# Kernel tuning notes

Measured on AMD Instinct MI355X. Metric: run time of the kernel, lower is better.

Reference implementation:

```python
import jax, jax.numpy as jnp
import numpy as np

# static config (matches init_kwargs / input_specs)
B, S, D, H, DH = 4, 2048, 2048, 16, 128
MAX_LEN = 1024  # round_up_to_multiple_of_256(max ragged length); lengths below max at 1024
ROPE_BASE = 10000.0


def setup_inputs() -> dict:
    key = jax.random.key(0)
    ks = jax.random.split(key, 8)
    q_src = jax.random.normal(ks[0], (B, MAX_LEN, D), jnp.float32)
    k_src = jax.random.normal(ks[1], (B, S, D), jnp.float32)
    v_src = jax.random.normal(ks[2], (B, S, D), jnp.float32)
    std = 1.0 / np.sqrt(D)
    Wq = jax.random.normal(ks[3], (D, H * DH), jnp.float32) * std
    Wk = jax.random.normal(ks[4], (D, H * DH), jnp.float32) * std
    Wv = jax.random.normal(ks[5], (D, H * DH), jnp.float32) * std
    Wo = jax.random.normal(ks[6], (H * DH, D), jnp.float32) * (1.0 / np.sqrt(H * DH))
    # mask[0]: causal bool [B,S,S]; mask[1]: full position ids [B,S]
    mask0 = jnp.broadcast_to(jnp.tril(jnp.ones((S, S), bool)), (B, S, S))
    pos_full = jnp.broadcast_to(jnp.arange(S, dtype=jnp.int32), (B, S))
    # ragged skip_mask: row i keeps lengths[i] random positions (max 1024 -> MAX_LEN)
    lengths = jnp.array([1024, 896, 768, 640], jnp.int32)
    scores = jax.random.uniform(ks[7], (B, S))
    ranks = jnp.argsort(jnp.argsort(scores, axis=1), axis=1)
    skip_mask = ranks < lengths[:, None]
    return {"q_src": q_src, "k_src": k_src, "v_src": v_src,
            "Wq": Wq, "Wk": Wk, "Wv": Wv, "Wo": Wo,
            "mask0": mask0, "pos_full": pos_full, "skip_mask": skip_mask}


def _rope(x, positions):
    # x: [B,H,L,DH], positions: [B,L] int -> rotary embedding on full head dim
    dh = x.shape[-1]
    inv_freq = 1.0 / (ROPE_BASE ** (jnp.arange(0, dh, 2, dtype=jnp.float32) / dh))
    freqs = positions.astype(jnp.float32)[:, :, None] * inv_freq      # [B,L,dh/2]
    emb = jnp.concatenate([freqs, freqs], axis=-1)[:, None]           # [B,1,L,dh]
    x1, x2 = jnp.split(x, 2, axis=-1)
    rot = jnp.concatenate([-x2, x1], axis=-1)                         # rotate_half
    return x * jnp.cos(emb) + rot * jnp.sin(emb)


def reference(q_src, k_src, v_src, Wq, Wk, Wv, Wo, mask0, pos_full, skip_mask):
    def heads(x, W):
        y = x @ W
        return y.reshape(x.shape[0], x.shape[1], H, DH).transpose(0, 2, 1, 3)

    q = heads(q_src, Wq)   # [B,H,MAX_LEN,DH]
    k = heads(k_src, Wk)   # [B,H,S,DH]
    v = heads(v_src, Wv)   # [B,H,S,DH]

    # _trim_attention_mask: gather kept rows (True-first, stable order), pad to MAX_LEN
    order = jnp.argsort(jnp.where(skip_mask, 0, 1), axis=1)[:, :MAX_LEN]  # [B,MAX_LEN]
    n = skip_mask.sum(axis=1)                                             # ragged lengths
    valid = jnp.arange(MAX_LEN)[None, :] < n[:, None]                     # [B,MAX_LEN]
    amask = jnp.take_along_axis(mask0, order[:, :, None], axis=1) & valid[:, :, None]
    pos_trim = jnp.where(valid, jnp.take_along_axis(pos_full, order, axis=1), 0)

    # RoPE: trimmed positions for q, full positions for k
    q = _rope(q, pos_trim)
    k = _rope(k, pos_full)

    # masked SDPA; fully-masked (padded) query rows -> zero output
    logits = jnp.einsum('bhld,bhsd->bhls', q, k) / np.sqrt(DH).astype(np.float32)
    logits = jnp.where(amask[:, None], logits, jnp.finfo(logits.dtype).min)
    probs = jax.nn.softmax(logits, axis=-1) * valid[:, None, :, None]
    ctx = jnp.einsum('bhls,bhsd->bhld', probs, v)                         # [B,H,MAX_LEN,DH]

    out = ctx.transpose(0, 2, 1, 3).reshape(B, MAX_LEN, H * DH) @ Wo     # [B,MAX_LEN,D]
    return out
```

## Files before the change

### kernel.cpp

```cpp
#include <hip/hip_runtime.h>

#define BB 4
#define SS 2048
#define DD 2048
#define HH 16
#define DHD 128
#define MAXL 1024

typedef __bf16 bf16x8 __attribute__((ext_vector_type(8)));
typedef float f32x4 __attribute__((ext_vector_type(4)));
typedef unsigned int u32_as1 __attribute__((address_space(1)));
typedef unsigned int u32_as3 __attribute__((address_space(3)));

__device__ __forceinline__ unsigned short f2bf(float f) {
  unsigned int u = __builtin_bit_cast(unsigned int, f);
  u += 0x7fffu + ((u >> 16) & 1u);
  return (unsigned short)(u >> 16);
}
__device__ __forceinline__ float bf2f(unsigned short h) {
  unsigned int u = ((unsigned int)h) << 16;
  return __builtin_bit_cast(float, u);
}
union U4 { uint4 u; bf16x8 b; };
__device__ __forceinline__ bf16x8 ldfrag(const unsigned short* p) {
  U4 x; x.u = *(const uint4*)p; return x.b;
}
__device__ __forceinline__ void gl_lds16(const void* g, void* l) {
  __builtin_amdgcn_global_load_lds((const u32_as1*)g, (u32_as3*)l, 16, 0, 0);
}

template <int C>
__device__ __forceinline__ float dppf(float x) {
  return __builtin_bit_cast(float,
      __builtin_amdgcn_mov_dpp(__builtin_bit_cast(int, x), C, 0xF, 0xF, true));
}
__device__ __forceinline__ float rmax16(float x) {
  x = fmaxf(x, dppf<0xB1>(x));
  x = fmaxf(x, dppf<0x4E>(x));
  x = fmaxf(x, dppf<0x141>(x));
  x = fmaxf(x, dppf<0x140>(x));
  return x;
}
__device__ __forceinline__ float radd16(float x) {
  x += dppf<0xB1>(x);
  x += dppf<0x4E>(x);
  x += dppf<0x141>(x);
  x += dppf<0x140>(x);
  return x;
}

#define NCVT 40960
#define NTW  4096
__global__ __launch_bounds__(256) void prep(
    const float* __restrict__ q, const float* __restrict__ k, const float* __restrict__ v,
    unsigned short* __restrict__ oq, unsigned short* __restrict__ ok,
    unsigned short* __restrict__ ov,
    const float* __restrict__ w0, const float* __restrict__ w1,
    const float* __restrict__ w2, const float* __restrict__ w3,
    unsigned short* __restrict__ t0, unsigned short* __restrict__ t1,
    unsigned short* __restrict__ t2, unsigned short* __restrict__ t3,
    const int* __restrict__ skip, int* __restrict__ posk, int* __restrict__ nval) {
  __shared__ __align__(16) unsigned short tile[64 * 76];
  __shared__ int cnts[64], offs[64];
  const int bid = blockIdx.x;
  const int tx = threadIdx.x;

  if (bid < NCVT) {
    const int nq = BB * MAXL * DD / 4, nk = BB * SS * DD / 4;
    int idx = bid * 256 + tx;
    const float* src; unsigned short* dst; int off;
    if (idx < nq) { src = q; dst = oq; off = idx; }
    else if (idx < nq + nk) { src = k; dst = ok; off = idx - nq; }
    else { src = v; dst = ov; off = idx - nq - nk; }
    float4 vv = ((const float4*)src)[off];
    ushort4 hh;
    hh.x = f2bf(vv.x); hh.y = f2bf(vv.y); hh.z = f2bf(vv.z); hh.w = f2bf(vv.w);
    ((ushort4*)dst)[off] = hh;
  } else if (bid < NCVT + NTW) {
    int rem = bid - NCVT;
    int z = rem >> 10, r2 = rem & 1023;
    int bx = r2 & 31, by = r2 >> 5;
    const float* W; unsigned short* Wt;
    switch (z) {
      case 0: W = w0; Wt = t0; break;
      case 1: W = w1; Wt = t1; break;
      case 2: W = w2; Wt = t2; break;
      default: W = w3; Wt = t3; break;
    }
    int K0 = by * 64, N0 = bx * 64;
    #pragma unroll
    for (int i = 0; i < 4; i++) {
      int r = (tx >> 4) + i * 16, c4 = (tx & 15) * 4;
      float4 vv = *(const float4*)&W[(size_t)(K0 + r) * DD + N0 + c4];
      ushort4 hh;
      hh.x = f2bf(vv.x); hh.y = f2bf(vv.y); hh.z = f2bf(vv.z); hh.w = f2bf(vv.w);
      *(ushort4*)&tile[r * 76 + c4] = hh;
    }
    __syncthreads();
    #pragma unroll
    for (int i = 0; i < 4; i++) {
      int n = (tx >> 4) + i * 16, k4 = (tx & 15) * 4;
      ushort4 hh;
      hh.x = tile[(k4 + 0) * 76 + n];
      hh.y = tile[(k4 + 1) * 76 + n];
      hh.z = tile[(k4 + 2) * 76 + n];
      hh.w = tile[(k4 + 3) * 76 + n];
      *(ushort4*)&Wt[(size_t)(N0 + n) * DD + K0 + k4] = hh;
    }
  } else {
    int b = bid - (NCVT + NTW);
    const int* row = skip + b * SS;
    if (tx < 64) {
      int c = 0;
      for (int i = 0; i < 32; i++) c += (row[tx * 32 + i] != 0);
      cnts[tx] = c;
    }
    __syncthreads();
    if (tx == 0) {
      int run = 0;
      for (int i = 0; i < 64; i++) { offs[i] = run; run += cnts[i]; }
      nval[b] = run > MAXL ? MAXL : run;
    }
    __syncthreads();
    if (tx < 64) {
      int o = offs[tx];
      for (int i = 0; i < 32; i++)
        if (row[tx * 32 + i]) { if (o < MAXL) posk[b * MAXL + o] = tx * 32 + i; o++; }
      int nb = nval[b];
      for (int l = nb + tx; l < MAXL; l += 64) posk[b * MAXL + l] = -1;
    }
  }
}

template <int BM>
__global__ __launch_bounds__(512, 2) void gemm8(const unsigned short* __restrict__ A,
                                                const unsigned short* __restrict__ Bt,
                                                void* __restrict__ Cp,
                                                int M, int N, int K, int mode, int Lbits) {
  constexpr int AW = BM * 64;
  __shared__ __align__(16) unsigned short lds[(BM + 256) * 64 * 2];
  unsigned short* const Abuf = lds;
  unsigned short* const Bbuf = lds + 2 * AW;

  const int tid = threadIdx.x;
  const int lane = tid & 63, quad = lane >> 4, c = lane & 15;
  const int w = tid >> 6;
  const int wm = (w >> 2) * (BM / 2), wn = (w & 3) * 64;

  const int nwg = gridDim.x * gridDim.y;
  const int bid0 = blockIdx.y * gridDim.x + blockIdx.x;
  const int cpx = nwg >> 3;
  const int bid = (bid0 & 7) * cpx + (bid0 >> 3);
  const int bx = bid % gridDim.x;
  const int by = bid / gridDim.x;
  const size_t tm = (size_t)by * BM, tn = (size_t)bx * 256;

  constexpr int MR = BM / 32;
  f32x4 acc[MR][4] = {};

  const int trow = tid >> 3;
  const int tch = ((tid & 7) ^ (trow & 7)) * 8;
  const unsigned short* gA = A + (tm + trow) * (size_t)K + tch;
  const unsigned short* gB = Bt + (tn + trow) * (size_t)K + tch;
  constexpr int ALD = BM / 64;
  constexpr int NLD = ALD + 4;

  auto STAGE = [&](int sel, int kk) {
    unsigned short* ad = Abuf + sel * AW;
    unsigned short* bd = Bbuf + sel * 16384;
    #pragma unroll
    for (int i = 0; i < ALD; i++)
      gl_lds16(gA + kk + (size_t)(i * 64) * K, ad + i * 4096 + tid * 8);
    #pragma unroll
    for (int i = 0; i < 4; i++)
      gl_lds16(gB + kk + (size_t)(i * 64) * K, bd + i * 4096 + tid * 8);
  };

  const int nkt = K >> 6;
  STAGE(0, 0);

  for (int t = 0; t < nkt; ++t) {
    const int sel = t & 1;
    const unsigned short* as = Abuf + sel * AW;
    const unsigned short* bs = Bbuf + sel * 16384;
    if (t + 1 < nkt) {
      STAGE(sel ^ 1, (t + 1) << 6);
      asm volatile("s_waitcnt vmcnt(%0)" ::"i"(NLD) : "memory");
    } else {
      asm volatile("s_waitcnt vmcnt(0)" ::: "memory");
    }
    __builtin_amdgcn_s_barrier();

    bf16x8 a0[4][2], b01[2][2], b23[2][2];
    #pragma unroll
    for (int i = 0; i < 4; i++)
      #pragma unroll
      for (int ks = 0; ks < 2; ks++)
        a0[i][ks] = ldfrag(&as[(wm + i * 16 + c) * 64 + (((ks * 4 + quad) ^ (c & 7)) << 3)]);
    #pragma unroll
    for (int j = 0; j < 2; j++)
      #pragma unroll
      for (int ks = 0; ks < 2; ks++)
        b01[j][ks] = ldfrag(&bs[(wn + j * 16 + c) * 64 + (((ks * 4 + quad) ^ (c & 7)) << 3)]);
    __builtin_amdgcn_s_barrier();
    __builtin_amdgcn_s_setprio(1);
    #pragma unroll
    for (int i = 0; i < 4; i++)
      #pragma unroll
      for (int j = 0; j < 2; j++)
        #pragma unroll
        for (int ks = 0; ks < 2; ks++)
          acc[i][j] = __builtin_amdgcn_mfma_f32_16x16x32_bf16(a0[i][ks], b01[j][ks], acc[i][j], 0, 0, 0);
    __builtin_amdgcn_s_setprio(0);
    __builtin_amdgcn_s_barrier();
    #pragma unroll
    for (int j = 0; j < 2; j++)
      #pragma unroll
      for (int ks = 0; ks < 2; ks++)
        b23[j][ks] = ldfrag(&bs[(wn + 32 + j * 16 + c) * 64 + (((ks * 4 + quad) ^ (c & 7)) << 3)]);
    __builtin_amdgcn_s_barrier();
    __builtin_amdgcn_s_setprio(1);
    #pragma unroll
    for (int i = 0; i < 4; i++)
      #pragma unroll
      for (int ks = 0; ks < 2; ks++)
        #pragma unroll
        for (int j = 0; j < 2; j++)
          acc[i][2 + j] = __builtin_amdgcn_mfma_f32_16x16x32_bf16(a0[i][ks], b23[j][ks], acc[i][2 + j], 0, 0, 0);
    __builtin_amdgcn_s_setprio(0);
    __builtin_amdgcn_s_barrier();

    if constexpr (BM == 256) {
      bf16x8 a1[4][2];
      #pragma unroll
      for (int i = 0; i < 4; i++)
        #pragma unroll
        for (int ks = 0; ks < 2; ks++)
          a1[i][ks] = ldfrag(&as[(wm + 64 + i * 16 + c) * 64 + (((ks * 4 + quad) ^ (c & 7)) << 3)]);
      __builtin_amdgcn_s_barrier();
      __builtin_amdgcn_s_setprio(1);
      #pragma unroll
      for (int i = 0; i < 4; i++)
        #pragma unroll
        for (int j = 0; j < 2; j++)
          #pragma unroll
          for (int ks = 0; ks < 2; ks++)
            acc[4 + i][j] = __builtin_amdgcn_mfma_f32_16x16x32_bf16(a1[i][ks], b01[j][ks], acc[4 + i][j], 0, 0, 0);
      __builtin_amdgcn_s_setprio(0);
      __builtin_amdgcn_s_barrier();
      __builtin_amdgcn_s_setprio(1);
      #pragma unroll
      for (int i = 0; i < 4; i++)
        #pragma unroll
        for (int j = 0; j < 2; j++)
          #pragma unroll
          for (int ks = 0; ks < 2; ks++)
            acc[4 + i][2 + j] = __builtin_amdgcn_mfma_f32_16x16x32_bf16(a1[i][ks], b23[j][ks], acc[4 + i][2 + j], 0, 0, 0);
      __builtin_amdgcn_s_setprio(0);
      __builtin_amdgcn_s_barrier();
    }
  }

  if (mode == 1) {
    float* Cf = (float*)Cp;
    #pragma unroll
    for (int i = 0; i < MR; i++)
      #pragma unroll
      for (int j = 0; j < 4; j++)
        #pragma unroll
        for (int r = 0; r < 4; r++) {
          size_t m = tm + wm + i * 16 + quad * 4 + r;
          size_t n = tn + wn + j * 16 + c;
          Cf[m * N + n] = acc[i][j][r];
        }
    return;
  }
  unsigned short* Cb = (unsigned short*)Cp;
  unsigned short* ep = lds + w * 4352;
  constexpr int MH = BM / 128;
  if (mode == 0) {
    const size_t Lmask = ((size_t)1 << Lbits) - 1;
    #pragma unroll
    for (int mh = 0; mh < MH; mh++) {
      #pragma unroll
      for (int i = 0; i < 4; i++)
        #pragma unroll
        for (int j = 0; j < 4; j++)
          #pragma unroll
          for (int r = 0; r < 4; r++)
            ep[(i * 16 + quad * 4 + r) * 68 + j * 16 + c] = f2bf(acc[mh * 4 + i][j][r]);
      #pragma unroll
      for (int it = 0; it < 8; it++) {
        int chunk = it * 64 + lane;
        int ml = chunk >> 3, nc = (chunk & 7) * 8;
        uint4 val = *(const uint4*)&ep[ml * 68 + nc];
        size_t m = tm + wm + mh * 64 + ml, n = tn + wn + nc;
        size_t b = m >> Lbits, l = m & Lmask, h = n >> 7, d = n & 127;
        *(uint4*)&Cb[(((b * HH + h) << Lbits) + l) * 128 + d] = val;
      }
    }
  } else {
    #pragma unroll
    for (int mh = 0; mh < MH; mh++) {
      #pragma unroll
      for (int i = 0; i < 4; i++)
        #pragma unroll
        for (int j = 0; j < 4; j++)
          #pragma unroll
          for (int r = 0; r < 4; r++)
            ep[(j * 16 + c) * 68 + i * 16 + quad * 4 + r] = f2bf(acc[mh * 4 + i][j][r]);
      #pragma unroll
      for (int it = 0; it < 8; it++) {
        int chunk = it * 64 + lane;
        int nl = chunk >> 3, mc = (chunk & 7) * 8;
        uint4 val = *(const uint4*)&ep[nl * 68 + mc];
        size_t n = tn + wn + nl, m = tm + wm + mh * 64 + mc;
        size_t b = m >> 11, s = m & 2047, h = n >> 7, d = n & 127;
        *(uint4*)&Cb[((b * HH + h) * 128 + d) * SS + s] = val;
      }
    }
  }
}

__global__ __launch_bounds__(256) void rope2(unsigned short* __restrict__ xq,
                                             unsigned short* __restrict__ xk,
                                             const int* __restrict__ posk) {
  constexpr float QSCL = (float)(0.08838834764831843 * 1.4426950408889634);
  const int Nq = BB * HH * MAXL * 64;
  int gid = blockIdx.x * 256 + threadIdx.x;
  unsigned short* x; int Lbits, idx, use_posk;
  if (gid < Nq) { x = xq; Lbits = 10; use_posk = 1; idx = gid; }
  else { x = xk; Lbits = 11; use_posk = 0; idx = gid - Nq; }
  int d = idx & 63;
  int rest = idx >> 6;
  int l = rest & ((1 << Lbits) - 1);
  int bh = rest >> Lbits;
  int b = bh >> 4;
  int p = use_posk ? posk[(b << 10) + l] : l;
  float ang = (float)p * __expf(-(float)d * 0.14391156831212787f);
  float sn, cs;
  __sincosf(ang, &sn, &cs);
  float S = use_posk ? QSCL : 1.0f;
  size_t base = (size_t)rest * 128;
  float x1 = bf2f(x[base + d]), x2 = bf2f(x[base + d + 64]);
  x[base + d]      = f2bf((x1 * cs - x2 * sn) * S);
  x[base + d + 64] = f2bf((x2 * cs + x1 * sn) * S);
}

__global__ __launch_bounds__(256) void attn_kernel(const unsigned short* __restrict__ qp,
                                                   const unsigned short* __restrict__ kp,
                                                   const unsigned short* __restrict__ vtp,
                                                   const int* __restrict__ posk,
                                                   const int* __restrict__ nval,
                                                   unsigned short* __restrict__ ctx) {
  __shared__ __align__(16) unsigned short k_s[2][64 * 128];
  __shared__ __align__(16) unsigned short vt_s[2][128 * 64];
  __shared__ __align__(16) unsigned short p_s[4 * 16 * 72];
  __shared__ int km_s[128];

  const int tid = threadIdx.x;
  const int w = tid >> 6, lane = tid & 63, quad = lane >> 4, c = lane & 15;
  const int bh = blockIdx.x, b = bh >> 4, h = bh & 15;
  const int qbase = blockIdx.y << 7;
  const int nb = nval[b];

  if (tid < 128) {
    int l = qbase + tid;
    km_s[tid] = (l < nb) ? posk[(b << 10) + l] : -1;
  }
  __syncthreads();

  int lv = nb - 1 - qbase; lv = lv > 127 ? 127 : lv;
  const int nkt = (lv >= 0) ? ((km_s[lv] >> 6) + 1) : 0;

  int wkx[2], kmn[2], km[2][4];
  #pragma unroll
  for (int s = 0; s < 2; s++) {
    int bs = s * 64 + w * 16;
    bool whas = (bs <= lv);
    int wl = bs + 15; if (wl > lv) wl = lv;
    wkx[s] = whas ? km_s[wl] : -1;
    kmn[s] = whas ? km_s[bs] : -1;
    #pragma unroll
    for (int r = 0; r < 4; r++) km[s][r] = km_s[bs + quad * 4 + r];
  }

  const unsigned short* qg = qp + ((size_t)bh << 10) * 128;
  bf16x8 aq[2][4];
  #pragma unroll
  for (int s = 0; s < 2; s++)
    #pragma unroll
    for (int ks = 0; ks < 4; ks++)
      aq[s][ks] = ldfrag(&qg[(size_t)(qbase + s * 64 + w * 16 + c) * 128 + ks * 32 + quad * 8]);
  asm volatile("" : "+v"(aq[0][0]), "+v"(aq[0][1]), "+v"(aq[0][2]), "+v"(aq[0][3]),
                    "+v"(aq[1][0]), "+v"(aq[1][1]), "+v"(aq[1][2]), "+v"(aq[1][3]) :: "memory");

  const int srow = tid >> 4;
  const int kswz = (tid & 15) ^ (srow & 7);
  const unsigned short* kgp = kp + ((size_t)bh << 11) * 128 + (size_t)srow * 128 + kswz * 8;
  const int dvrow = tid >> 3;
  const int vswz = (tid & 7) ^ (dvrow & 7);
  const unsigned short* vgp = vtp + ((size_t)bh * 128 + dvrow) * SS + vswz * 8;

  auto STG = [&](int buf, int kb) {
    #pragma unroll
    for (int i = 0; i < 4; i++)
      gl_lds16(kgp + ((size_t)kb + i * 16) * 128, &k_s[buf][(i * 256 + tid) * 8]);
    #pragma unroll
    for (int i = 0; i < 4; i++)
      gl_lds16(vgp + (size_t)kb + (size_t)i * 32 * SS, &vt_s[buf][(i * 256 + tid) * 8]);
  };

  float m_i[2][4], l_i[2][4];
  #pragma unroll
  for (int s = 0; s < 2; s++)
    #pragma unroll
    for (int r = 0; r < 4; r++) { m_i[s][r] = -1e30f; l_i[s][r] = 0.f; }
  f32x4 o[2][8];
  #pragma unroll
  for (int s = 0; s < 2; s++)
    #pragma unroll
    for (int dj = 0; dj < 8; dj++) o[s][dj] = (f32x4){0.f, 0.f, 0.f, 0.f};

  if (nkt > 0) STG(0, 0);

  for (int kt = 0; kt < nkt; kt++) {
    const int cur = kt & 1;
    const int kb = kt * 64;
    if (kt + 1 < nkt) {
      STG(cur ^ 1, kb + 64);
      asm volatile("s_waitcnt vmcnt(8)" ::: "memory");
    } else {
      asm volatile("s_waitcnt vmcnt(0)" ::: "memory");
    }
    __builtin_amdgcn_s_barrier();

    #pragma unroll
    for (int s = 0; s < 2; s++) {
      if (kb <= wkx[s]) {
        f32x4 sa[4];
        #pragma unroll
        for (int j = 0; j < 4; j++) {
          sa[j] = (f32x4){0.f, 0.f, 0.f, 0.f};
          #pragma unroll
          for (int ks = 0; ks < 4; ks++) {
            bf16x8 bk = ldfrag(&k_s[cur][((j * 16 + c) << 7) + (((ks * 4 + quad) ^ (c & 7)) << 3)]);
            sa[j] = __builtin_amdgcn_mfma_f32_16x16x32_bf16(aq[s][ks], bk, sa[j], 0, 0, 0);
          }
        }

        float mt[4] = {-1e30f, -1e30f, -1e30f, -1e30f};
        if (kb + 63 <= kmn[s]) {
          #pragma unroll
          for (int j = 0; j < 4; j++)
            #pragma unroll
            for (int r = 0; r < 4; r++) mt[r] = fmaxf(mt[r], sa[j][r]);
        } else {
          #pragma unroll
          for (int j = 0; j < 4; j++) {
            int key = kb + j * 16 + c;
            #pragma unroll
            for (int r = 0; r < 4; r++) {
              float v = (key <= km[s][r]) ? sa[j][r] : -1e30f;
              sa[j][r] = v;
              mt[r] = fmaxf(mt[r], v);
            }
          }
        }
        float al[4], rs[4];
        #pragma unroll
        for (int r = 0; r < 4; r++) {
          mt[r] = rmax16(mt[r]);
          float mn = fmaxf(m_i[s][r], mt[r]);
          al[r] = __builtin_exp2f(m_i[s][r] - mn);
          m_i[s][r] = mn;
          rs[r] = 0.f;
        }
        #pragma unroll
        for (int j = 0; j < 4; j++)
          #pragma unroll
          for (int r = 0; r < 4; r++) {
            float pv = __builtin_exp2f(sa[j][r] - m_i[s][r]);
            sa[j][r] = pv;
            rs[r] += pv;
          }
        #pragma unroll
        for (int r = 0; r < 4; r++) {
          rs[r] = radd16(rs[r]);
          l_i[s][r] = l_i[s][r] * al[r] + rs[r];
        }
        #pragma unroll
        for (int dj = 0; dj < 8; dj++)
          #pragma unroll
          for (int r = 0; r < 4; r++) o[s][dj][r] *= al[r];

        #pragma unroll
        for (int j = 0; j < 4; j++)
          #pragma unroll
          for (int r = 0; r < 4; r++)
            p_s[w * 1152 + (quad * 4 + r) * 72 + j * 16 + c] = f2bf(sa[j][r]);

        #pragma unroll
        for (int ks2 = 0; ks2 < 2; ks2++) {
          bf16x8 ap = ldfrag(&p_s[w * 1152 + c * 72 + ks2 * 32 + quad * 8]);
          #pragma unroll
          for (int dj = 0; dj < 8; dj++) {
            bf16x8 bv = ldfrag(&vt_s[cur][((dj * 16 + c) << 6) + (((ks2 * 4 + quad) ^ (c & 7)) << 3)]);
            o[s][dj] = __builtin_amdgcn_mfma_f32_16x16x32_bf16(ap, bv, o[s][dj], 0, 0, 0);
          }
        }
      }
    }
    __builtin_amdgcn_s_barrier();
  }

  #pragma unroll
  for (int s = 0; s < 2; s++)
    #pragma unroll
    for (int r = 0; r < 4; r++) {
      int l = qbase + s * 64 + w * 16 + quad * 4 + r;
      bool ok = (l < nb);
      float inv = ok ? (1.0f / l_i[s][r]) : 0.0f;
      #pragma unroll
      for (int dj = 0; dj < 8; dj++)
        ctx[(((size_t)b << 10) + l) * (size_t)DD + h * 128 + dj * 16 + c] =
            f2bf(ok ? o[s][dj][r] * inv : 0.0f);
    }
}

extern "C" void kernel_launch(void* const* d_in, const int* in_sizes, int n_in,
                              void* d_out, int out_size, void* d_ws, size_t ws_size,
                              hipStream_t stream) {
  const float* q_src = (const float*)d_in[0];
  const float* k_src = (const float*)d_in[1];
  const float* v_src = (const float*)d_in[2];
  const float* Wq = (const float*)d_in[3];
  const float* Wk = (const float*)d_in[4];
  const float* Wv = (const float*)d_in[5];
  const float* Wo = (const float*)d_in[6];
  const int* skip = (const int*)d_in[9];

  char* p = (char*)d_ws;
  auto alloc = [&](size_t bytes) -> char* {
    char* r = p;
    p += (bytes + 255) & ~(size_t)255;
    return r;
  };
  unsigned short* a_q  = (unsigned short*)alloc((size_t)BB * MAXL * DD * 2);
  unsigned short* a_k  = (unsigned short*)alloc((size_t)BB * SS * DD * 2);
  unsigned short* a_v  = (unsigned short*)alloc((size_t)BB * SS * DD * 2);
  unsigned short* wt_q = (unsigned short*)alloc((size_t)DD * DD * 2);
  unsigned short* wt_k = (unsigned short*)alloc((size_t)DD * DD * 2);
  unsigned short* wt_v = (unsigned short*)alloc((size_t)DD * DD * 2);
  unsigned short* wt_o = (unsigned short*)alloc((size_t)DD * DD * 2);
  unsigned short* q_pro = (unsigned short*)alloc((size_t)BB * HH * MAXL * DHD * 2);
  unsigned short* k_pro = (unsigned short*)alloc((size_t)BB * HH * SS * DHD * 2);
  unsigned short* v_t   = (unsigned short*)alloc((size_t)BB * HH * SS * DHD * 2);
  int* posk = (int*)alloc((size_t)BB * MAXL * 4);
  int* nval = (int*)alloc(64);
  unsigned short* ctx = a_q;

  prep<<<NCVT + NTW + BB, 256, 0, stream>>>(q_src, k_src, v_src, a_q, a_k, a_v,
                                            Wq, Wk, Wv, Wo, wt_q, wt_k, wt_v, wt_o,
                                            skip, posk, nval);

  gemm8<128><<<dim3(8, 32), 512, 0, stream>>>(a_q, wt_q, q_pro, BB * MAXL, DD, DD, 0, 10);
  gemm8<256><<<dim3(8, 32), 512, 0, stream>>>(a_k, wt_k, k_pro, BB * SS, DD, DD, 0, 11);
  gemm8<256><<<dim3(8, 32), 512, 0, stream>>>(a_v, wt_v, v_t, BB * SS, DD, DD, 2, 11);

  rope2<<<(BB * HH * (MAXL + SS) * 64) / 256, 256, 0, stream>>>(q_pro, k_pro, posk);

  attn_kernel<<<dim3(BB * HH, MAXL / 128), 256, 0, stream>>>(q_pro, k_pro, v_t, posk, nval, ctx);

  gemm8<128><<<dim3(8, 32), 512, 0, stream>>>(ctx, wt_o, d_out, BB * MAXL, DD, DD, 1, 0);
}
```

Before: 709.6 us.

## Merge Q/K/V projection GEMMs into one launch and shrink attention query tile

The three projection GEMMs become a single kernel with 640 workgroups of 256x256 tiles. Each workgroup picks its Q, K or V operands from its row-block index, which removes two launch boundaries and fills the GPU better than three separate grids. The attention kernel now uses 64-query tiles instead of 128 across twice as many blocks. It single-buffers K and V and prefetches them in a split K-then-V schedule, aiming for more parallelism and less LDS at the cost of less data reuse per K tile. The output GEMM becomes a dedicated fp32-output kernel.

New measurement: 731.6 us. +3.1%, slower.

```diff
diff --git a/kernel.cpp b/kernel.cpp
--- a/kernel.cpp
+++ b/kernel.cpp
@@ -132,20 +132,195 @@
   }
 }
 
-template <int BM>
-__global__ __launch_bounds__(512, 2) void gemm8(const unsigned short* __restrict__ A,
-                                                const unsigned short* __restrict__ Bt,
-                                                void* __restrict__ Cp,
-                                                int M, int N, int K, int mode, int Lbits) {
-  constexpr int AW = BM * 64;
-  __shared__ __align__(16) unsigned short lds[(BM + 256) * 64 * 2];
+__global__ __launch_bounds__(512, 2) void gemm_proj(
+    const unsigned short* __restrict__ Aq, const unsigned short* __restrict__ Bq,
+    unsigned short* __restrict__ Cq,
+    const unsigned short* __restrict__ Ak, const unsigned short* __restrict__ Bk,
+    unsigned short* __restrict__ Ck,
+    const unsigned short* __restrict__ Av, const unsigned short* __restrict__ Bv,
+    unsigned short* __restrict__ Cv) {
+  constexpr int K = DD;
+  __shared__ __align__(16) unsigned short lds[65536];
   unsigned short* const Abuf = lds;
-  unsigned short* const Bbuf = lds + 2 * AW;
+  unsigned short* const Bbuf = lds + 32768;
 
   const int tid = threadIdx.x;
   const int lane = tid & 63, quad = lane >> 4, c = lane & 15;
   const int w = tid >> 6;
-  const int wm = (w >> 2) * (BM / 2), wn = (w & 3) * 64;
+  const int wm = (w >> 2) * 128, wn = (w & 3) * 64;
+
+  const int nwg = gridDim.x * gridDim.y;
+  const int bid0 = blockIdx.y * gridDim.x + blockIdx.x;
+  const int cpx = nwg >> 3;
+  const int bid = (bid0 & 7) * cpx + (bid0 >> 3);
+  const int bx = bid & 7;
+  const int by = bid >> 3;
+
+  const unsigned short *A, *Bt;
+  unsigned short* Cout;
+  int mode, Lbits, lby;
+  if (by < 16)      { A = Aq; Bt = Bq; Cout = Cq; mode = 0; Lbits = 10; lby = by; }
+  else if (by < 48) { A = Ak; Bt = Bk; Cout = Ck; mode = 0; Lbits = 11; lby = by - 16; }
+  else              { A = Av; Bt = Bv; Cout = Cv; mode = 2; Lbits = 11; lby = by - 48; }
+  const size_t tm = (size_t)lby * 256, tn = (size_t)bx * 256;
+
+  f32x4 acc[8][4] = {};
+
+  const int trow = tid >> 3;
+  const int tch = ((tid & 7) ^ (trow & 7)) * 8;
+  const unsigned short* gA = A + (tm + trow) * (size_t)K + tch;
+  const unsigned short* gB = Bt + (tn + trow) * (size_t)K + tch;
+
+  auto STAGE = [&](int sel, int kk) {
+    unsigned short* ad = Abuf + sel * 16384;
+    unsigned short* bd = Bbuf + sel * 16384;
+    #pragma unroll
+    for (int i = 0; i < 4; i++)
+      gl_lds16(gA + kk + (size_t)(i * 64) * K, ad + i * 4096 + tid * 8);
+    #pragma unroll
+    for (int i = 0; i < 4; i++)
+      gl_lds16(gB + kk + (size_t)(i * 64) * K, bd + i * 4096 + tid * 8);
+  };
+
+  const int nkt = K >> 6;
+  STAGE(0, 0);
+
+  for (int t = 0; t < nkt; ++t) {
+    const int sel = t & 1;
+    const unsigned short* as = Abuf + sel * 16384;
+    const unsigned short* bs = Bbuf + sel * 16384;
+    if (t + 1 < nkt) {
+      STAGE(sel ^ 1, (t + 1) << 6);
+      asm volatile("s_waitcnt vmcnt(8)" ::: "memory");
+    } else {
+      asm volatile("s_waitcnt vmcnt(0)" ::: "memory");
+    }
+    __builtin_amdgcn_s_barrier();
+
+    bf16x8 a0[4][2], b01[2][2], b23[2][2];
+    #pragma unroll
+    for (int i = 0; i < 4; i++)
+      #pragma unroll
+      for (int ks = 0; ks < 2; ks++)
+        a0[i][ks] = ldfrag(&as[(wm + i * 16 + c) * 64 + (((ks * 4 + quad) ^ (c & 7)) << 3)]);
+    #pragma unroll
+    for (int j = 0; j < 2; j++)
+      #pragma unroll
+      for (int ks = 0; ks < 2; ks++)
+        b01[j][ks] = ldfrag(&bs[(wn + j * 16 + c) * 64 + (((ks * 4 + quad) ^ (c & 7)) << 3)]);
+    __builtin_amdgcn_s_barrier();
+    __builtin_amdgcn_s_setprio(1);
+    #pragma unroll
+    for (int i = 0; i < 4; i++)
+      #pragma unroll
+      for (int j = 0; j < 2; j++)
+        #pragma unroll
+        for (int ks = 0; ks < 2; ks++)
+          acc[i][j] = __builtin_amdgcn_mfma_f32_16x16x32_bf16(a0[i][ks], b01[j][ks], acc[i][j], 0, 0, 0);
+    __builtin_amdgcn_s_setprio(0);
+    __builtin_amdgcn_s_barrier();
+    #pragma unroll
+    for (int j = 0; j < 2; j++)
+      #pragma unroll
+      for (int ks = 0; ks < 2; ks++)
+        b23[j][ks] = ldfrag(&bs[(wn + 32 + j * 16 + c) * 64 + (((ks * 4 + quad) ^ (c & 7)) << 3)]);
+    __builtin_amdgcn_s_barrier();
+    __builtin_amdgcn_s_setprio(1);
+    #pragma unroll
+    for (int i = 0; i < 4; i++)
+      #pragma unroll
+      for (int j = 0; j < 2; j++)
+        #pragma unroll
+        for (int ks = 0; ks < 2; ks++)
+          acc[i][2 + j] = __builtin_amdgcn_mfma_f32_16x16x32_bf16(a0[i][ks], b23[j][ks], acc[i][2 + j], 0, 0, 0);
+    __builtin_amdgcn_s_setprio(0);
+    __builtin_amdgcn_s_barrier();
+    bf16x8 a1[4][2];
+    #pragma unroll
+    for (int i = 0; i < 4; i++)
+      #pragma unroll
+      for (int ks = 0; ks < 2; ks++)
+        a1[i][ks] = ldfrag(&as[(wm + 64 + i * 16 + c) * 64 + (((ks * 4 + quad) ^ (c & 7)) << 3)]);
+    __builtin_amdgcn_s_barrier();
+    __builtin_amdgcn_s_setprio(1);
+    #pragma unroll
+    for (int i = 0; i < 4; i++)
+      #pragma unroll
+      for (int j = 0; j < 2; j++)
+        #pragma unroll
+        for (int ks = 0; ks < 2; ks++)
+          acc[4 + i][j] = __builtin_amdgcn_mfma_f32_16x16x32_bf16(a1[i][ks], b01[j][ks], acc[4 + i][j], 0, 0, 0);
+    __builtin_amdgcn_s_setprio(0);
+    __builtin_amdgcn_s_barrier();
+    __builtin_amdgcn_s_setprio(1);
+    #pragma unroll
+    for (int i = 0; i < 4; i++)
+      #pragma unroll
+      for (int j = 0; j < 2; j++)
+        #pragma unroll
+        for (int ks = 0; ks < 2; ks++)
+          acc[4 + i][2 + j] = __builtin_amdgcn_mfma_f32_16x16x32_bf16(a1[i][ks], b23[j][ks], acc[4 + i][2 + j], 0, 0, 0);
+    __builtin_amdgcn_s_setprio(0);
+    __builtin_amdgcn_s_barrier();
+  }
+
+  unsigned short* ep = lds + w * 4352;
+  const size_t Lmask = ((size_t)1 << Lbits) - 1;
+  if (mode == 0) {
+    #pragma unroll
+    for (int mh = 0; mh < 2; mh++) {
+      #pragma unroll
+      for (int i = 0; i < 4; i++)
+        #pragma unroll
+        for (int j = 0; j < 4; j++)
+          #pragma unroll
+          for (int r = 0; r < 4; r++)
+            ep[(i * 16 + quad * 4 + r) * 68 + j * 16 + c] = f2bf(acc[mh * 4 + i][j][r]);
+      #pragma unroll
+      for (int it = 0; it < 8; it++) {
+        int chunk = it * 64 + lane;
+        int ml = chunk >> 3, nc = (chunk & 7) * 8;
+        uint4 val = *(const uint4*)&ep[ml * 68 + nc];
+        size_t m = tm + wm + mh * 64 + ml, n = tn + wn + nc;
+        size_t b = m >> Lbits, l = m & Lmask, h = n >> 7, d = n & 127;
+        *(uint4*)&Cout[(((b * HH + h) << Lbits) + l) * 128 + d] = val;
+      }
+    }
+  } else {
+    #pragma unroll
+    for (int mh = 0; mh < 2; mh++) {
+      #pragma unroll
+      for (int i = 0; i < 4; i++)
+        #pragma unroll
+        for (int j = 0; j < 4; j++)
+          #pragma unroll
+          for (int r = 0; r < 4; r++)
+            ep[(j * 16 + c) * 68 + i * 16 + quad * 4 + r] = f2bf(acc[mh * 4 + i][j][r]);
+      #pragma unroll
+      for (int it = 0; it < 8; it++) {
+        int chunk = it * 64 + lane;
+        int nl = chunk >> 3, mc = (chunk & 7) * 8;
+        uint4 val = *(const uint4*)&ep[nl * 68 + mc];
+        size_t n = tn + wn + nl, m = tm + wm + mh * 64 + mc;
+        size_t b = m >> 11, s = m & 2047, h = n >> 7, d = n & 127;
+        *(uint4*)&Cout[((b * HH + h) * 128 + d) * SS + s] = val;
+      }
+    }
+  }
+}
+
+__global__ __launch_bounds__(512, 2) void gemm_o(const unsigned short* __restrict__ A,
+                                                 const unsigned short* __restrict__ Bt,
+                                                 float* __restrict__ Cf,
+                                                 int M, int N, int K) {
+  __shared__ __align__(16) unsigned short lds[(128 + 256) * 64 * 2];
+  unsigned short* const Abuf = lds;
+  unsigned short* const Bbuf = lds + 16384;
+
+  const int tid = threadIdx.x;
+  const int lane = tid & 63, quad = lane >> 4, c = lane & 15;
+  const int w = tid >> 6;
+  const int wm = (w >> 2) * 64, wn = (w & 3) * 64;
 
   const int nwg = gridDim.x * gridDim.y;
   const int bid0 = blockIdx.y * gridDim.x + blockIdx.x;
@@ -153,23 +328,20 @@
   const int bid = (bid0 & 7) * cpx + (bid0 >> 3);
   const int bx = bid % gridDim.x;
   const int by = bid / gridDim.x;
-  const size_t tm = (size_t)by * BM, tn = (size_t)bx * 256;
-
-  constexpr int MR = BM / 32;
-  f32x4 acc[MR][4] = {};
+  const size_t tm = (size_t)by * 128, tn = (size_t)bx * 256;
+
+  f32x4 acc[4][4] = {};
 
   const int trow = tid >> 3;
   const int tch = ((tid & 7) ^ (trow & 7)) * 8;
   const unsigned short* gA = A + (tm + trow) * (size_t)K + tch;
   const unsigned short* gB = Bt + (tn + trow) * (size_t)K + tch;
-  constexpr int ALD = BM / 64;
-  constexpr int NLD = ALD + 4;
 
   auto STAGE = [&](int sel, int kk) {
-    unsigned short* ad = Abuf + sel * AW;
+    unsigned short* ad = Abuf + sel * 8192;
     unsigned short* bd = Bbuf + sel * 16384;
     #pragma unroll
-    for (int i = 0; i < ALD; i++)
+    for (int i = 0; i < 2; i++)
       gl_lds16(gA + kk + (size_t)(i * 64) * K, ad + i * 4096 + tid * 8);
     #pragma unroll
     for (int i = 0; i < 4; i++)
@@ -181,11 +353,11 @@
 
   for (int t = 0; t < nkt; ++t) {
     const int sel = t & 1;
-    const unsigned short* as = Abuf + sel * AW;
+    const unsigned short* as = Abuf + sel * 8192;
     const unsigned short* bs = Bbuf + sel * 16384;
     if (t + 1 < nkt) {
       STAGE(sel ^ 1, (t + 1) << 6);
-      asm volatile("s_waitcnt vmcnt(%0)" ::"i"(NLD) : "memory");
+      asm volatile("s_waitcnt vmcnt(6)" ::: "memory");
     } else {
       asm volatile("s_waitcnt vmcnt(0)" ::: "memory");
     }
@@ -223,103 +395,24 @@
     #pragma unroll
     for (int i = 0; i < 4; i++)
       #pragma unroll
-      for (int ks = 0; ks < 2; ks++)
-        #pragma unroll
-        for (int j = 0; j < 2; j++)
+      for (int j = 0; j < 2; j++)
+        #pragma unroll
+        for (int ks = 0; ks < 2; ks++)
           acc[i][2 + j] = __builtin_amdgcn_mfma_f32_16x16x32_bf16(a0[i][ks], b23[j][ks], acc[i][2 + j], 0, 0, 0);
     __builtin_amdgcn_s_setprio(0);
     __builtin_amdgcn_s_barrier();
-
-    if constexpr (BM == 256) {
-      bf16x8 a1[4][2];
-      #pragma unroll
-      for (int i = 0; i < 4; i++)
-        #pragma unroll
-        for (int ks = 0; ks < 2; ks++)
-          a1[i][ks] = ldfrag(&as[(wm + 64 + i * 16 + c) * 64 + (((ks * 4 + quad) ^ (c & 7)) << 3)]);
-      __builtin_amdgcn_s_barrier();
-      __builtin_amdgcn_s_setprio(1);
-      #pragma unroll
-      for (int i = 0; i < 4; i++)
-        #pragma unroll
-        for (int j = 0; j < 2; j++)
-          #pragma unroll
-          for (int ks = 0; ks < 2; ks++)
-            acc[4 + i][j] = __builtin_amdgcn_mfma_f32_16x16x32_bf16(a1[i][ks], b01[j][ks], acc[4 + i][j], 0, 0, 0);
-      __builtin_amdgcn_s_setprio(0);
-      __builtin_amdgcn_s_barrier();
-      __builtin_amdgcn_s_setprio(1);
-      #pragma unroll
-      for (int i = 0; i < 4; i++)
-        #pragma unroll
-        for (int j = 0; j < 2; j++)
-          #pragma unroll
-          for (int ks = 0; ks < 2; ks++)
-            acc[4 + i][2 + j] = __builtin_amdgcn_mfma_f32_16x16x32_bf16(a1[i][ks], b23[j][ks], acc[4 + i][2 + j], 0, 0, 0);
-      __builtin_amdgcn_s_setprio(0);
-      __builtin_amdgcn_s_barrier();
-    }
   }
 
-  if (mode == 1) {
-    float* Cf = (float*)Cp;
-    #pragma unroll
-    for (int i = 0; i < MR; i++)
-      #pragma unroll
-      for (int j = 0; j < 4; j++)
-        #pragma unroll
-        for (int r = 0; r < 4; r++) {
-          size_t m = tm + wm + i * 16 + quad * 4 + r;
-          size_t n = tn + wn + j * 16 + c;
-          Cf[m * N + n] = acc[i][j][r];
-        }
-    return;
-  }
-  unsigned short* Cb = (unsigned short*)Cp;
-  unsigned short* ep = lds + w * 4352;
-  constexpr int MH = BM / 128;
-  if (mode == 0) {
-    const size_t Lmask = ((size_t)1 << Lbits) - 1;
-    #pragma unroll
-    for (int mh = 0; mh < MH; mh++) {
-      #pragma unroll
-      for (int i = 0; i < 4; i++)
-        #pragma unroll
-        for (int j = 0; j < 4; j++)
-          #pragma unroll
-          for (int r = 0; r < 4; r++)
-            ep[(i * 16 + quad * 4 + r) * 68 + j * 16 + c] = f2bf(acc[mh * 4 + i][j][r]);
-      #pragma unroll
-      for (int it = 0; it < 8; it++) {
-        int chunk = it * 64 + lane;
-        int ml = chunk >> 3, nc = (chunk & 7) * 8;
-        uint4 val = *(const uint4*)&ep[ml * 68 + nc];
-        size_t m = tm + wm + mh * 64 + ml, n = tn + wn + nc;
-        size_t b = m >> Lbits, l = m & Lmask, h = n >> 7, d = n & 127;
-        *(uint4*)&Cb[(((b * HH + h) << Lbits) + l) * 128 + d] = val;
-      }
-    }
-  } else {
-    #pragma unroll
-    for (int mh = 0; mh < MH; mh++) {
-      #pragma unroll
-      for (int i = 0; i < 4; i++)
-        #pragma unroll
-        for (int j = 0; j < 4; j++)
-          #pragma unroll
-          for (int r = 0; r < 4; r++)
-            ep[(j * 16 + c) * 68 + i * 16 + quad * 4 + r] = f2bf(acc[mh * 4 + i][j][r]);
-      #pragma unroll
-      for (int it = 0; it < 8; it++) {
-        int chunk = it * 64 + lane;
-        int nl = chunk >> 3, mc = (chunk & 7) * 8;
-        uint4 val = *(const uint4*)&ep[nl * 68 + mc];
-        size_t n = tn + wn + nl, m = tm + wm + mh * 64 + mc;
-        size_t b = m >> 11, s = m & 2047, h = n >> 7, d = n & 127;
-        *(uint4*)&Cb[((b * HH + h) * 128 + d) * SS + s] = val;
-      }
-    }
-  }
+  #pragma unroll
+  for (int i = 0; i < 4; i++)
+    #pragma unroll
+    for (int j = 0; j < 4; j++)
+      #pragma unroll
+      for (int r = 0; r < 4; r++) {
+        size_t m = tm + wm + i * 16 + quad * 4 + r;
+        size_t n = tn + wn + j * 16 + c;
+        Cf[m * N + n] = acc[i][j][r];
+      }
 }
 
 __global__ __launch_bounds__(256) void rope2(unsigned short* __restrict__ xq,
@@ -353,47 +446,40 @@
                                                    const int* __restrict__ posk,
                                                    const int* __restrict__ nval,
                                                    unsigned short* __restrict__ ctx) {
-  __shared__ __align__(16) unsigned short k_s[2][64 * 128];
-  __shared__ __align__(16) unsigned short vt_s[2][128 * 64];
+  __shared__ __align__(16) unsigned short k_s[64 * 128];
+  __shared__ __align__(16) unsigned short vt_s[128 * 64];
   __shared__ __align__(16) unsigned short p_s[4 * 16 * 72];
-  __shared__ int km_s[128];
+  __shared__ int km_s[64];
 
   const int tid = threadIdx.x;
   const int w = tid >> 6, lane = tid & 63, quad = lane >> 4, c = lane & 15;
   const int bh = blockIdx.x, b = bh >> 4, h = bh & 15;
-  const int qbase = blockIdx.y << 7;
+  const int qbase = blockIdx.y * 64;
   const int nb = nval[b];
 
-  if (tid < 128) {
+  if (tid < 64) {
     int l = qbase + tid;
     km_s[tid] = (l < nb) ? posk[(b << 10) + l] : -1;
   }
   __syncthreads();
 
-  int lv = nb - 1 - qbase; lv = lv > 127 ? 127 : lv;
-  const int nkt = (lv >= 0) ? ((km_s[lv] >> 6) + 1) : 0;
-
-  int wkx[2], kmn[2], km[2][4];
+  int lv = nb - 1 - qbase; lv = lv > 63 ? 63 : lv;
+  const int tile_kmax = (lv >= 0) ? km_s[lv] : -1;
+  const int nkt = (tile_kmax >= 0) ? ((tile_kmax >> 6) + 1) : 0;
+  const bool whas = (w * 16 <= lv);
+  int wl = w * 16 + 15; if (wl > lv) wl = lv;
+  const int wkmax = whas ? km_s[wl] : -1;
+  const int kminw = whas ? km_s[w * 16] : -1;
+  int km[4];
   #pragma unroll
-  for (int s = 0; s < 2; s++) {
-    int bs = s * 64 + w * 16;
-    bool whas = (bs <= lv);
-    int wl = bs + 15; if (wl > lv) wl = lv;
-    wkx[s] = whas ? km_s[wl] : -1;
-    kmn[s] = whas ? km_s[bs] : -1;
-    #pragma unroll
-    for (int r = 0; r < 4; r++) km[s][r] = km_s[bs + quad * 4 + r];
-  }
-
-  const unsigned short* qg = qp + ((size_t)bh << 10) * 128;
-  bf16x8 aq[2][4];
+  for (int r = 0; r < 4; r++) km[r] = km_s[w * 16 + quad * 4 + r];
+
+  const unsigned short* qg = qp + (((size_t)bh << 10) + qbase) * 128;
+  bf16x8 aq[4];
   #pragma unroll
-  for (int s = 0; s < 2; s++)
-    #pragma unroll
-    for (int ks = 0; ks < 4; ks++)
-      aq[s][ks] = ldfrag(&qg[(size_t)(qbase + s * 64 + w * 16 + c) * 128 + ks * 32 + quad * 8]);
-  asm volatile("" : "+v"(aq[0][0]), "+v"(aq[0][1]), "+v"(aq[0][2]), "+v"(aq[0][3]),
-                    "+v"(aq[1][0]), "+v"(aq[1][1]), "+v"(aq[1][2]), "+v"(aq[1][3]) :: "memory");
+  for (int ks = 0; ks < 4; ks++)
+    aq[ks] = ldfrag(&qg[(size_t)(w * 16 + c) * 128 + ks * 32 + quad * 8]);
+  asm volatile("" : "+v"(aq[0]), "+v"(aq[1]), "+v"(aq[2]), "+v"(aq[3]) :: "memory");
 
   const int srow = tid >> 4;
   const int kswz = (tid & 15) ^ (srow & 7);
@@ -402,130 +488,130 @@
   const int vswz = (tid & 7) ^ (dvrow & 7);
   const unsigned short* vgp = vtp + ((size_t)bh * 128 + dvrow) * SS + vswz * 8;
 
-  auto STG = [&](int buf, int kb) {
-    #pragma unroll
-    for (int i = 0; i < 4; i++)
-      gl_lds16(kgp + ((size_t)kb + i * 16) * 128, &k_s[buf][(i * 256 + tid) * 8]);
-    #pragma unroll
-    for (int i = 0; i < 4; i++)
-      gl_lds16(vgp + (size_t)kb + (size_t)i * 32 * SS, &vt_s[buf][(i * 256 + tid) * 8]);
+  auto STG_K = [&](int kb) {
+    #pragma unroll
+    for (int i = 0; i < 4; i++)
+      gl_lds16(kgp + ((size_t)kb + i * 16) * 128, &k_s[(i * 256 + tid) * 8]);
   };
-
-  float m_i[2][4], l_i[2][4];
+  auto STG_V = [&](int kb) {
+    #pragma unroll
+    for (int i = 0; i < 4; i++)
+      gl_lds16(vgp + (size_t)kb + (size_t)i * 32 * SS, &vt_s[(i * 256 + tid) * 8]);
+  };
+
+  float m_i[4], l_i[4];
   #pragma unroll
-  for (int s = 0; s < 2; s++)
-    #pragma unroll
-    for (int r = 0; r < 4; r++) { m_i[s][r] = -1e30f; l_i[s][r] = 0.f; }
-  f32x4 o[2][8];
+  for (int r = 0; r < 4; r++) { m_i[r] = -1e30f; l_i[r] = 0.f; }
+  f32x4 o[8];
   #pragma unroll
-  for (int s = 0; s < 2; s++)
-    #pragma unroll
-    for (int dj = 0; dj < 8; dj++) o[s][dj] = (f32x4){0.f, 0.f, 0.f, 0.f};
-
-  if (nkt > 0) STG(0, 0);
+  for (int dj = 0; dj < 8; dj++) o[dj] = (f32x4){0.f, 0.f, 0.f, 0.f};
+
+  if (nkt > 0) { STG_K(0); STG_V(0); }
 
   for (int kt = 0; kt < nkt; kt++) {
-    const int cur = kt & 1;
     const int kb = kt * 64;
-    if (kt + 1 < nkt) {
-      STG(cur ^ 1, kb + 64);
-      asm volatile("s_waitcnt vmcnt(8)" ::: "memory");
-    } else {
-      asm volatile("s_waitcnt vmcnt(0)" ::: "memory");
-    }
-    __builtin_amdgcn_s_barrier();
-
-    #pragma unroll
-    for (int s = 0; s < 2; s++) {
-      if (kb <= wkx[s]) {
-        f32x4 sa[4];
+    const bool more = (kt + 1 < nkt);
+    const bool act = (kb <= wkmax);
+
+    asm volatile("s_waitcnt vmcnt(4)" ::: "memory");
+    __builtin_amdgcn_s_barrier();
+
+    f32x4 sa[4];
+    if (act) {
+      #pragma unroll
+      for (int j = 0; j < 4; j++) {
+        sa[j] = (f32x4){0.f, 0.f, 0.f, 0.f};
+        #pragma unroll
+        for (int ks = 0; ks < 4; ks++) {
+          bf16x8 bk = ldfrag(&k_s[((j * 16 + c) << 7) + (((ks * 4 + quad) ^ (c & 7)) << 3)]);
+          sa[j] = __builtin_amdgcn_mfma_f32_16x16x32_bf16(aq[ks], bk, sa[j], 0, 0, 0);
+        }
+      }
+    }
+    __builtin_amdgcn_s_barrier();
+    if (more) STG_K(kb + 64);
+
+    if (act) {
+      float mt[4] = {-1e30f, -1e30f, -1e30f, -1e30f};
+      if (kb + 63 <= kminw) {
+        #pragma unroll
+        for (int j = 0; j < 4; j++)
+          #pragma unroll
+          for (int r = 0; r < 4; r++) mt[r] = fmaxf(mt[r], sa[j][r]);
+      } else {
         #pragma unroll
         for (int j = 0; j < 4; j++) {
-          sa[j] = (f32x4){0.f, 0.f, 0.f, 0.f};
+          int key = kb + j * 16 + c;
           #pragma unroll
-          for (int ks = 0; ks < 4; ks++) {
-            bf16x8 bk = ldfrag(&k_s[cur][((j * 16 + c) << 7) + (((ks * 4 + quad) ^ (c & 7)) << 3)]);
-            sa[j] = __builtin_amdgcn_mfma_f32_16x16x32_bf16(aq[s][ks], bk, sa[j], 0, 0, 0);
+          for (int r = 0; r < 4; r++) {
+            float v = (key <= km[r]) ? sa[j][r] : -1e30f;
+            sa[j][r] = v;
+            mt[r] = fmaxf(mt[r], v);
           }
         }
-
-        float mt[4] = {-1e30f, -1e30f, -1e30f, -1e30f};
-        if (kb + 63 <= kmn[s]) {
-          #pragma unroll
-          for (int j = 0; j < 4; j++)
-            #pragma unroll
-            for (int r = 0; r < 4; r++) mt[r] = fmaxf(mt[r], sa[j][r]);
-        } else {
-          #pragma unroll
-          for (int j = 0; j < 4; j++) {
-            int key = kb + j * 16 + c;
-            #pragma unroll
-            for (int r = 0; r < 4; r++) {
-              float v = (key <= km[s][r]) ? sa[j][r] : -1e30f;
-              sa[j][r] = v;
-              mt[r] = fmaxf(mt[r], v);
-            }
-          }
+      }
+      float al[4], rs[4];
+      #pragma unroll
+      for (int r = 0; r < 4; r++) {
+        mt[r] = rmax16(mt[r]);
+        float mn = fmaxf(m_i[r], mt[r]);
+        al[r] = __builtin_exp2f(m_i[r] - mn);
+        m_i[r] = mn;
+        rs[r] = 0.f;
+      }
+      #pragma unroll
+      for (int j = 0; j < 4; j++)
+        #pragma unroll
+        for (int r = 0; r < 4; r++) {
+          float pv = __builtin_exp2f(sa[j][r] - m_i[r]);
+          sa[j][r] = pv;
+          rs[r] += pv;
         }
-        float al[4], rs[4];
-        #pragma unroll
-        for (int r = 0; r < 4; r++) {
-          mt[r] = rmax16(mt[r]);
-          float mn = fmaxf(m_i[s][r], mt[r]);
-          al[r] = __builtin_exp2f(m_i[s][r] - mn);
-          m_i[s][r] = mn;
-          rs[r] = 0.f;
+      #pragma unroll
+      for (int r = 0; r < 4; r++) {
+        rs[r] = radd16(rs[r]);
+        l_i[r] = l_i[r] * al[r] + rs[r];
+      }
+      #pragma unroll
+      for (int dj = 0; dj < 8; dj++)
+        #pragma unroll
+        for (int r = 0; r < 4; r++) o[dj][r] *= al[r];
+    }
+
+    if (more) { asm volatile("s_waitcnt vmcnt(4)" ::: "memory"); }
+    else      { asm volatile("s_waitcnt vmcnt(0)" ::: "memory"); }
+    __builtin_amdgcn_s_barrier();
+
+    if (act) {
+      #pragma unroll
+      for (int j = 0; j < 4; j++)
+        #pragma unroll
+        for (int r = 0; r < 4; r++)
+          p_s[w * 1152 + (quad * 4 + r) * 72 + j * 16 + c] = f2bf(sa[j][r]);
+      #pragma unroll
+      for (int ks2 = 0; ks2 < 2; ks2++) {
+        bf16x8 ap = ldfrag(&p_s[w * 1152 + c * 72 + ks2 * 32 + quad * 8]);
+        #pragma unroll
+        for (int dj = 0; dj < 8; dj++) {
+          bf16x8 bv = ldfrag(&vt_s[((dj * 16 + c) << 6) + (((ks2 * 4 + quad) ^ (c & 7)) << 3)]);
+          o[dj] = __builtin_amdgcn_mfma_f32_16x16x32_bf16(ap, bv, o[dj], 0, 0, 0);
         }
-        #pragma unroll
-        for (int j = 0; j < 4; j++)
-          #pragma unroll
-          for (int r = 0; r < 4; r++) {
-            float pv = __builtin_exp2f(sa[j][r] - m_i[s][r]);
-            sa[j][r] = pv;
-            rs[r] += pv;
-          }
-        #pragma unroll
-        for (int r = 0; r < 4; r++) {
-          rs[r] = radd16(rs[r]);
-          l_i[s][r] = l_i[s][r] * al[r] + rs[r];
-        }
-        #pragma unroll
-        for (int dj = 0; dj < 8; dj++)
-          #pragma unroll
-          for (int r = 0; r < 4; r++) o[s][dj][r] *= al[r];
-
-        #pragma unroll
-        for (int j = 0; j < 4; j++)
-          #pragma unroll
-          for (int r = 0; r < 4; r++)
-            p_s[w * 1152 + (quad * 4 + r) * 72 + j * 16 + c] = f2bf(sa[j][r]);
-
-        #pragma unroll
-        for (int ks2 = 0; ks2 < 2; ks2++) {
-          bf16x8 ap = ldfrag(&p_s[w * 1152 + c * 72 + ks2 * 32 + quad * 8]);
-          #pragma unroll
-          for (int dj = 0; dj < 8; dj++) {
-            bf16x8 bv = ldfrag(&vt_s[cur][((dj * 16 + c) << 6) + (((ks2 * 4 + quad) ^ (c & 7)) << 3)]);
-            o[s][dj] = __builtin_amdgcn_mfma_f32_16x16x32_bf16(ap, bv, o[s][dj], 0, 0, 0);
-          }
-        }
-      }
-    }
-    __builtin_amdgcn_s_barrier();
+      }
+    }
+    __builtin_amdgcn_s_barrier();
+    if (more) STG_V(kb + 64);
   }
 
   #pragma unroll
-  for (int s = 0; s < 2; s++)
-    #pragma unroll
-    for (int r = 0; r < 4; r++) {
-      int l = qbase + s * 64 + w * 16 + quad * 4 + r;
-      bool ok = (l < nb);
-      float inv = ok ? (1.0f / l_i[s][r]) : 0.0f;
-      #pragma unroll
-      for (int dj = 0; dj < 8; dj++)
-        ctx[(((size_t)b << 10) + l) * (size_t)DD + h * 128 + dj * 16 + c] =
-            f2bf(ok ? o[s][dj][r] * inv : 0.0f);
-    }
+  for (int r = 0; r < 4; r++) {
+    int l = qbase + w * 16 + quad * 4 + r;
+    bool ok = (l < nb);
+    float inv = ok ? (1.0f / l_i[r]) : 0.0f;
+    #pragma unroll
+    for (int dj = 0; dj < 8; dj++)
+      ctx[(((size_t)b << 10) + l) * (size_t)DD + h * 128 + dj * 16 + c] =
+          f2bf(ok ? o[dj][r] * inv : 0.0f);
+  }
 }
 
 extern "C" void kernel_launch(void* const* d_in, const int* in_sizes, int n_in,
@@ -564,13 +650,13 @@
                                             Wq, Wk, Wv, Wo, wt_q, wt_k, wt_v, wt_o,
                                             skip, posk, nval);
 
-  gemm8<128><<<dim3(8, 32), 512, 0, stream>>>(a_q, wt_q, q_pro, BB * MAXL, DD, DD, 0, 10);
-  gemm8<256><<<dim3(8, 32), 512, 0, stream>>>(a_k, wt_k, k_pro, BB * SS, DD, DD, 0, 11);
-  gemm8<256><<<dim3(8, 32), 512, 0, stream>>>(a_v, wt_v, v_t, BB * SS, DD, DD, 2, 11);
+  gemm_proj<<<dim3(8, 80), 512, 0, stream>>>(a_q, wt_q, q_pro,
+                                             a_k, wt_k, k_pro,
+                                             a_v, wt_v, v_t);
 
   rope2<<<(BB * HH * (MAXL + SS) * 64) / 256, 256, 0, stream>>>(q_pro, k_pro, posk);
 
-  attn_kernel<<<dim3(BB * HH, MAXL / 128), 256, 0, stream>>>(q_pro, k_pro, v_t, posk, nval, ctx);
-
-  gemm8<128><<<dim3(8, 32), 512, 0, stream>>>(ctx, wt_o, d_out, BB * MAXL, DD, DD, 1, 0);
-}
+  attn_kernel<<<dim3(BB * HH, MAXL / 64), 256, 0, stream>>>(q_pro, k_pro, v_t, posk, nval, ctx);
+
+  gemm_o<<<dim3(8, 32), 512, 0, stream>>>(ctx, wt_o, (float*)d_out, BB * MAXL, DD, DD);
+}
```
